# Kernel tuning notes

Measured on AMD Instinct MI355X. Metric: run time of the kernel, lower is better.

## Reference

```python
import jax, jax.numpy as jnp
import numpy as np

C = 256
GROUPS = 32
EPS = 1e-6


def setup_inputs() -> dict:
    key = jax.random.key(0)
    ks = jax.random.split(key, 11)
    b, c, h, w, d = 4, C, 16, 16, 16
    s = 0.02
    return {
        "x": jax.random.normal(ks[0], (b, c, h, w, d), jnp.float32),
        "gn_w": jnp.ones((c,), jnp.float32),
        "gn_b": jnp.zeros((c,), jnp.float32),
        "wq": jax.random.normal(ks[1], (c, c), jnp.float32) * s,
        "bq": jnp.zeros((c,), jnp.float32),
        "wk": jax.random.normal(ks[2], (c, c), jnp.float32) * s,
        "bk": jnp.zeros((c,), jnp.float32),
        "wv": jax.random.normal(ks[3], (c, c), jnp.float32) * s,
        "bv": jnp.zeros((c,), jnp.float32),
        "wo": jax.random.normal(ks[4], (c, c), jnp.float32) * s,
        "bo": jnp.zeros((c,), jnp.float32),
    }


def group_norm(x, w, b):
    bsz, c, h, wd, d = x.shape
    xg = x.reshape(bsz, GROUPS, c // GROUPS, h, wd, d)
    mean = xg.mean(axis=(2, 3, 4, 5), keepdims=True)
    var = xg.var(axis=(2, 3, 4, 5), keepdims=True)
    xg = (xg - mean) * jax.lax.rsqrt(var + EPS)
    x = xg.reshape(bsz, c, h, wd, d)
    return x * w[None, :, None, None, None] + b[None, :, None, None, None]


def conv1(x, w, b):
    # 1x1x1 conv == channel-mixing matmul; x: [b,c,h,w,d], w: [out,in]
    return jnp.einsum('oc,bchwd->bohwd', w, x) + b[None, :, None, None, None]


def reference(x, gn_w, gn_b, wq, bq, wk, bk, wv, bv, wo, bo):
    b, c, h, w, d = x.shape
    scale = c ** (-0.5)
    xn = group_norm(x, gn_w, gn_b)
    q = conv1(xn, wq, bq).reshape(b, c, h * w * d)
    k = conv1(xn, wk, bk).reshape(b, c, h * w * d)
    v = conv1(xn, wv, bv).reshape(b, c, h * w * d)
    attn = jnp.einsum('bci,bcj->bij', q, k) * scale  # [b, N, N]
    attn = jax.nn.softmax(attn, axis=2)
    out = jnp.einsum('bij,bcj->bci', attn, v).reshape(b, c, h, w, d)
    out = conv1(out, wo, bo)
    return x + out
```

## Files before the change

### kernel.cpp

```cpp
#include <hip/hip_runtime.h>
#include <hip/hip_bf16.h>

#define BB 4
#define CC 256
#define NN 4096
#define BBNN (BB * NN)
#define NGROUPS 32
#define CPG 8
#define EPSG 1e-6f
#define QKSCL 0.30028063f
#define KSPLIT 4
#define JITERS (NN / KSPLIT / 64)
#define KSTRIDE 272
#define DEFER_THR 8.0f

#define SIGMA(c) (((c) & 0xC0) | (((c) & 0x18) << 1) | (((c) & 0x20) >> 2) | ((c) & 7))

typedef __bf16 bf16x8 __attribute__((ext_vector_type(8)));
typedef float  f32x4  __attribute__((ext_vector_type(4)));

typedef __attribute__((address_space(1))) const void g_void;
typedef __attribute__((address_space(3))) void l_void;

__device__ __forceinline__ unsigned short f2bf(float f) {
  unsigned u = __builtin_bit_cast(unsigned, f);
  u += 0x7fffu + ((u >> 16) & 1u);
  return (unsigned short)(u >> 16);
}
__device__ __forceinline__ float bf2f(unsigned short s) {
  return __builtin_bit_cast(float, (unsigned)s << 16);
}

__device__ __forceinline__ f32x4 mfma16(bf16x8 a, bf16x8 b, f32x4 c) {
  return __builtin_amdgcn_mfma_f32_16x16x32_bf16(a, b, c, 0, 0, 0);
}
__device__ __forceinline__ f32x4 mfma8(long a, long b, f32x4 c) {
  return __builtin_amdgcn_mfma_f32_16x16x32_fp8_fp8(a, b, c, 0, 0, 0);
}

__device__ __forceinline__ bf16x8 ldfrag(const unsigned short* p) {
  return __builtin_bit_cast(bf16x8, *(const uint4*)p);
}

__global__ __launch_bounds__(256) void pre(const float* __restrict__ wq,
    const float* __restrict__ wk, const float* __restrict__ wv,
    const float* __restrict__ wo, const float* __restrict__ x,
    unsigned short* __restrict__ wbf, float* __restrict__ part) {
  if (blockIdx.x < 256) {
    int mat = blockIdx.x >> 6, blk = blockIdx.x & 63;
    const float* s = mat == 0 ? wq : mat == 1 ? wk : mat == 2 ? wv : wo;
    int i = (blk * 256 + threadIdx.x) * 4;
    float4 v = *(const float4*)&s[i];
    unsigned short* d = wbf + (size_t)mat * CC * CC + i;
    d[0] = f2bf(v.x); d[1] = f2bf(v.y); d[2] = f2bf(v.z); d[3] = f2bf(v.w);
    return;
  }
  int bx = blockIdx.x - 256;
  int pair = bx >> 1, h = bx & 1;
  const float* xp = x + (size_t)pair * (CPG * NN) + (size_t)h * (CPG * NN / 2);
  float s = 0.f, s2 = 0.f;
  for (int i = threadIdx.x; i < CPG * NN / 8; i += 256) {
    float4 v = ((const float4*)xp)[i];
    s += v.x + v.y + v.z + v.w;
    s2 += v.x * v.x + v.y * v.y + v.z * v.z + v.w * v.w;
  }
  for (int o = 32; o; o >>= 1) { s += __shfl_down(s, o); s2 += __shfl_down(s2, o); }
  __shared__ float rs[4], rs2[4];
  int wid = threadIdx.x >> 6, lane = threadIdx.x & 63;
  if (lane == 0) { rs[wid] = s; rs2[wid] = s2; }
  __syncthreads();
  if (threadIdx.x == 0) {
    part[bx * 2 + 0] = rs[0] + rs[1] + rs[2] + rs[3];
    part[bx * 2 + 1] = rs2[0] + rs2[1] + rs2[2] + rs2[3];
  }
}

__global__ __launch_bounds__(512) void gqkv(const float* __restrict__ x,
    const float* __restrict__ gw, const float* __restrict__ gb,
    const float* __restrict__ part, const unsigned short* __restrict__ wbf,
    const float* __restrict__ bq, const float* __restrict__ bk,
    const float* __restrict__ bv,
    unsigned char* __restrict__ q8, unsigned char* __restrict__ k8,
    unsigned char* __restrict__ v8) {
  const int low = blockIdx.x & 7;
  const int b = low & 3, shalf = low >> 2;
  const int u = blockIdx.x >> 3;
  const int sidx = (u >> 4) * 2 + shalf;
  const int nt = sidx * 16 + (u & 15);
  const int n0 = nt * 64;
  __shared__ unsigned short Xs[64][CC + 8];
  int tid = threadIdx.x;
  const float* xb = x + (size_t)b * CC * NN;
  {
    int item = tid;
    int g = item >> 4, nc = item & 15;
    int pair = b * NGROUPS + g;
    float s = part[pair * 4 + 0] + part[pair * 4 + 2];
    float s2 = part[pair * 4 + 1] + part[pair * 4 + 3];
    float mean = s / (CPG * NN);
    float inv = rsqrtf(s2 / (CPG * NN) - mean * mean + EPSG);
    unsigned short row[4][8];
#pragma unroll
    for (int cc = 0; cc < 8; ++cc) {
      int c = g * 8 + cc;
      float wv = gw[c];
      float scv = inv * wv;
      float biv = gb[c] - mean * scv;
      float4 v = *(const float4*)&xb[(size_t)c * NN + n0 + nc * 4];
      row[0][cc] = f2bf(v.x * scv + biv);
      row[1][cc] = f2bf(v.y * scv + biv);
      row[2][cc] = f2bf(v.z * scv + biv);
      row[3][cc] = f2bf(v.w * scv + biv);
    }
#pragma unroll
    for (int r = 0; r < 4; ++r)
      *(uint4*)&Xs[nc * 4 + r][g * 8] = *(const uint4*)&row[r][0];
  }
  __syncthreads();
  int w = tid >> 6, lane = tid & 63;
  int m = lane & 15, q4 = lane >> 4;
  int mode = w >> 2, wsub = w & 3;
  {
    bf16x8 xa[8];
#pragma unroll
    for (int k = 0; k < 8; ++k)
      xa[k] = ldfrag(&Xs[wsub * 16 + m][k * 32 + q4 * 8]);
    const unsigned short* W = wbf + (size_t)mode * CC * CC;
    const float* bias = mode ? bk : bq;
    unsigned char* dst = mode ? k8 : q8;
    for (int ot = 0; ot < 16; ++ot) {
      f32x4 acc = {0.f, 0.f, 0.f, 0.f};
#pragma unroll
      for (int k = 0; k < 8; ++k) {
        bf16x8 bf = ldfrag(&W[(size_t)(ot * 16 + m) * CC + k * 32 + q4 * 8]);
        acc = mfma16(xa[k], bf, acc);
      }
      int o = ot * 16 + m;
      int so = SIGMA(o);
      float bia = bias[o];
      unsigned pk01 = __builtin_amdgcn_cvt_pk_fp8_f32(
          (acc[0] + bia) * QKSCL, (acc[1] + bia) * QKSCL, 0u, false);
      unsigned pk23 = __builtin_amdgcn_cvt_pk_fp8_f32(
          (acc[2] + bia) * QKSCL, (acc[3] + bia) * QKSCL, 0u, false);
      size_t base = ((size_t)b * NN + n0 + wsub * 16 + q4 * 4) * CC + so;
      dst[base]          = (unsigned char)(pk01 & 0xff);
      dst[base + CC]     = (unsigned char)((pk01 >> 8) & 0xff);
      dst[base + 2 * CC] = (unsigned char)(pk23 & 0xff);
      dst[base + 3 * CC] = (unsigned char)((pk23 >> 8) & 0xff);
    }
  }
  {
    const unsigned short* Wv = wbf + 2 * CC * CC;
    int nthalf = w >> 2;
    for (int ot = 0; ot < 4; ++ot) {
      int o0 = (w & 3) * 64 + ot * 16;
      bf16x8 af[8];
#pragma unroll
      for (int k = 0; k < 8; ++k)
        af[k] = ldfrag(&Wv[(size_t)(o0 + m) * CC + k * 32 + q4 * 8]);
#pragma unroll
      for (int hh = 0; hh < 2; ++hh) {
        int nt4 = nthalf * 2 + hh;
        f32x4 acc = {0.f, 0.f, 0.f, 0.f};
#pragma unroll
        for (int k = 0; k < 8; ++k) {
          bf16x8 bfr = ldfrag(&Xs[nt4 * 16 + m][k * 32 + q4 * 8]);
          acc = mfma16(af[k], bfr, acc);
        }
        int j = nt4 * 16 + m;
        int jp = (j & 0x23) | ((j & 0x0C) << 1) | ((j & 0x10) >> 2);
        int n = n0 + jp;
        int o = o0 + q4 * 4;
        unsigned pk01 = __builtin_amdgcn_cvt_pk_fp8_f32(acc[0] + bv[o], acc[1] + bv[o + 1], 0u, false);
        unsigned pk23 = __builtin_amdgcn_cvt_pk_fp8_f32(acc[2] + bv[o + 2], acc[3] + bv[o + 3], 0u, false);
        size_t base = ((size_t)b * CC + o) * NN + n;
        v8[base]          = (unsigned char)(pk01 & 0xff);
        v8[base + NN]     = (unsigned char)((pk01 >> 8) & 0xff);
        v8[base + 2 * NN] = (unsigned char)(pk23 & 0xff);
        v8[base + 3 * NN] = (unsigned char)((pk23 >> 8) & 0xff);
      }
    }
  }
}

__device__ __forceinline__ void stageK8(const unsigned char* __restrict__ kp,
    int j0, unsigned char* Kb, int tid) {
#pragma unroll
  for (int t = 0; t < 4; ++t) {
    int item = t * 256 + tid;
    int row = item / 17, g = item % 17;
    int gs = (g == 16) ? 0 : g;
    const unsigned char* gp = kp + (size_t)(j0 + row) * CC + gs * 16;
    __builtin_amdgcn_global_load_lds((g_void*)gp, (l_void*)(Kb + item * 16), 16, 0, 0);
  }
  if (tid < 64) {
    int item = 1024 + tid;
    int row = item / 17, g = item % 17;
    int gs = (g == 16) ? 0 : g;
    const unsigned char* gp = kp + (size_t)(j0 + row) * CC + gs * 16;
    __builtin_amdgcn_global_load_lds((g_void*)gp, (l_void*)(Kb + item * 16), 16, 0, 0);
  }
}
__device__ __forceinline__ void stageV8(const unsigned char* __restrict__ vp,
    int j0, unsigned char* Vb, int tid) {
#pragma unroll
  for (int t = 0; t < 4; ++t) {
    int item = t * 256 + tid;
    int row = item >> 2, gl = item & 3;
    int gg = gl ^ (row & 3);
    const unsigned char* g = vp + (size_t)row * NN + j0 + gg * 16;
    __builtin_amdgcn_global_load_lds((g_void*)g, (l_void*)(Vb + item * 16), 16, 0, 0);
  }
}

__global__ __launch_bounds__(256, 2) void attn(const unsigned char* __restrict__ q8,
    const unsigned char* __restrict__ k8, const unsigned char* __restrict__ v8,
    unsigned short* __restrict__ accP, float* __restrict__ mlP) {
  const int grp = blockIdx.x & 15;
  const int s = grp >> 2, b = grp & 3;
  const int it = blockIdx.x >> 4;
  const int i0 = it * 128;
  __shared__ __align__(16) unsigned char pool[67584];
  unsigned char* Kd0 = pool;
  unsigned char* Kd1 = pool + 17408;
  unsigned char* Vd0 = pool + 34816;
  unsigned char* Vd1 = pool + 51200;
  int tid = threadIdx.x, w = tid >> 6, lane = tid & 63;
  int m = lane & 15, q4 = lane >> 4;
  int q4h = q4 >> 1, q4l = q4 & 1;
  const unsigned char* kp = k8 + (size_t)b * NN * CC;
  const unsigned char* vp = v8 + (size_t)b * CC * NN;
  const int iA0 = i0 + w * 32;
  long qaA[8], qaB[8];
#pragma unroll
  for (int t = 0; t < 4; ++t) {
    uint4 va = *(const uint4*)&q8[((size_t)b * NN + iA0 + m) * CC + t * 64 + q4 * 16];
    uint4 vb = *(const uint4*)&q8[((size_t)b * NN + iA0 + 16 + m) * CC + t * 64 + q4 * 16];
    uint2 alo = {va.x, va.y}, ahi = {va.z, va.w};
    uint2 blo = {vb.x, vb.y}, bhi = {vb.z, vb.w};
    qaA[2 * t]     = __builtin_bit_cast(long, alo);
    qaA[2 * t + 1] = __builtin_bit_cast(long, ahi);
    qaB[2 * t]     = __builtin_bit_cast(long, blo);
    qaB[2 * t + 1] = __builtin_bit_cast(long, bhi);
  }
  f32x4 accA[16], accB[16];
#pragma unroll
  for (int i = 0; i < 16; ++i) {
    accA[i] = (f32x4){0.f, 0.f, 0.f, 0.f};
    accB[i] = (f32x4){0.f, 0.f, 0.f, 0.f};
  }
  float mrowA = -1e30f, lrowA = 0.f, mrowB = -1e30f, lrowB = 0.f;
  const int jbase = s * (NN / KSPLIT);
  stageK8(kp, jbase, Kd0, tid);
  stageV8(vp, jbase, Vd0, tid);
  const unsigned char* Kbase0 = Kd0 + m * KSTRIDE + q4 * 16;
  const unsigned char* Kbase1 = Kd1 + m * KSTRIDE + q4 * 16;
  for (int jt = 0; jt < JITERS; ++jt) {
    __syncthreads();
    const unsigned char* Kbase = (jt & 1) ? Kbase1 : Kbase0;
    const unsigned char* Vs    = (jt & 1) ? Vd1 : Vd0;
    f32x4 svA[4], svB[4];
    __builtin_amdgcn_s_setprio(1);
#pragma unroll
    for (int jt4 = 0; jt4 < 4; ++jt4) {
      f32x4 aA = {0.f, 0.f, 0.f, 0.f};
      f32x4 aB = {0.f, 0.f, 0.f, 0.f};
#pragma unroll
      for (int c16 = 0; c16 < 4; ++c16) {
        uint4 kq = *(const uint4*)&Kbase[jt4 * 16 * KSTRIDE + c16 * 64];
        uint2 l2 = {kq.x, kq.y}, h2 = {kq.z, kq.w};
        long klo = __builtin_bit_cast(long, l2);
        long khi = __builtin_bit_cast(long, h2);
        aA = mfma8(klo, qaA[2 * c16], aA);
        aB = mfma8(klo, qaB[2 * c16], aB);
        aA = mfma8(khi, qaA[2 * c16 + 1], aA);
        aB = mfma8(khi, qaB[2 * c16 + 1], aB);
      }
      svA[jt4] = aA;
      svB[jt4] = aB;
    }
    __builtin_amdgcn_s_setprio(0);
    if (jt + 1 < JITERS) {
      stageK8(kp, jbase + (jt + 1) * 64, (jt & 1) ? Kd0 : Kd1, tid);
      stageV8(vp, jbase + (jt + 1) * 64, (jt & 1) ? Vd0 : Vd1, tid);
    }
    float mxA = -1e30f, mxB = -1e30f;
#pragma unroll
    for (int jt4 = 0; jt4 < 4; ++jt4) {
      mxA = fmaxf(mxA, fmaxf(fmaxf(svA[jt4][0], svA[jt4][1]), fmaxf(svA[jt4][2], svA[jt4][3])));
      mxB = fmaxf(mxB, fmaxf(fmaxf(svB[jt4][0], svB[jt4][1]), fmaxf(svB[jt4][2], svB[jt4][3])));
    }
    mxA = fmaxf(mxA, __shfl_xor(mxA, 16));
    mxA = fmaxf(mxA, __shfl_xor(mxA, 32));
    mxB = fmaxf(mxB, __shfl_xor(mxB, 16));
    mxB = fmaxf(mxB, __shfl_xor(mxB, 32));
    if (__any(mxA - mrowA > DEFER_THR)) {
      float mnewA = fmaxf(mrowA, mxA);
      float alphaA = exp2f(mrowA - mnewA);
      mrowA = mnewA;
      lrowA *= alphaA;
#pragma unroll
      for (int ct = 0; ct < 16; ++ct) accA[ct] *= alphaA;
    }
    if (__any(mxB - mrowB > DEFER_THR)) {
      float mnewB = fmaxf(mrowB, mxB);
      float alphaB = exp2f(mrowB - mnewB);
      mrowB = mnewB;
      lrowB *= alphaB;
#pragma unroll
      for (int ct = 0; ct < 16; ++ct) accB[ct] *= alphaB;
    }
    float rsumA = 0.f, rsumB = 0.f;
    unsigned pdA[4], pdB[4];
#pragma unroll
    for (int jt4 = 0; jt4 < 4; ++jt4) {
      float e0 = exp2f(svA[jt4][0] - mrowA);
      float e1 = exp2f(svA[jt4][1] - mrowA);
      float e2 = exp2f(svA[jt4][2] - mrowA);
      float e3 = exp2f(svA[jt4][3] - mrowA);
      rsumA += (e0 + e1) + (e2 + e3);
      unsigned d = __builtin_amdgcn_cvt_pk_fp8_f32(e0, e1, 0u, false);
      pdA[jt4] = __builtin_amdgcn_cvt_pk_fp8_f32(e2, e3, d, true);
      float f0 = exp2f(svB[jt4][0] - mrowB);
      float f1 = exp2f(svB[jt4][1] - mrowB);
      float f2 = exp2f(svB[jt4][2] - mrowB);
      float f3 = exp2f(svB[jt4][3] - mrowB);
      rsumB += (f0 + f1) + (f2 + f3);
      unsigned e = __builtin_amdgcn_cvt_pk_fp8_f32(f0, f1, 0u, false);
      pdB[jt4] = __builtin_amdgcn_cvt_pk_fp8_f32(f2, f3, e, true);
    }
    rsumA += __shfl_xor(rsumA, 16);
    rsumA += __shfl_xor(rsumA, 32);
    rsumB += __shfl_xor(rsumB, 16);
    rsumB += __shfl_xor(rsumB, 32);
    lrowA += rsumA;
    lrowB += rsumB;
    int voff = ((q4h) ^ (m & 3)) * 16 + q4l * 8;
    int voff1 = ((2 + q4h) ^ (m & 3)) * 16 + q4l * 8;
    __builtin_amdgcn_s_setprio(1);
#pragma unroll
    for (int p = 0; p < 2; ++p) {
      uint2 puA = {pdA[2 * p], pdA[2 * p + 1]};
      uint2 puB = {pdB[2 * p], pdB[2 * p + 1]};
      long pTA = __builtin_bit_cast(long, puA);
      long pTB = __builtin_bit_cast(long, puB);
      int vo = p ? voff1 : voff;
#pragma unroll
      for (int ct = 0; ct < 16; ++ct) {
        long vf = *(const long*)&Vs[(ct * 16 + m) * 64 + vo];
        accA[ct] = mfma8(vf, pTA, accA[ct]);
        accB[ct] = mfma8(vf, pTB, accB[ct]);
      }
    }
    __builtin_amdgcn_s_setprio(0);
  }
  size_t rqA = (size_t)(s * BB + b) * NN + iA0 + m;
  if (q4 == 0) {
    mlP[rqA * 2 + 0] = mrowA;
    mlP[rqA * 2 + 1] = lrowA;
    mlP[(rqA + 16) * 2 + 0] = mrowB;
    mlP[(rqA + 16) * 2 + 1] = lrowB;
  }
  __syncthreads();
  unsigned short* tp = (unsigned short*)pool;
#pragma unroll
  for (int half = 0; half < 2; ++half) {
    if ((w >> 1) == half) {
      int rbase = (w & 1) * 32;
#pragma unroll
      for (int ct = 0; ct < 16; ++ct) {
        unsigned loA = f2bf(accA[ct][0]) | ((unsigned)f2bf(accA[ct][1]) << 16);
        unsigned hiA = f2bf(accA[ct][2]) | ((unsigned)f2bf(accA[ct][3]) << 16);
        uint2 pkA = {loA, hiA};
        *(uint2*)&tp[(rbase + m) * 260 + ct * 16 + q4 * 4] = pkA;
        unsigned loB = f2bf(accB[ct][0]) | ((unsigned)f2bf(accB[ct][1]) << 16);
        unsigned hiB = f2bf(accB[ct][2]) | ((unsigned)f2bf(accB[ct][3]) << 16);
        uint2 pkB = {loB, hiB};
        *(uint2*)&tp[(rbase + 16 + m) * 260 + ct * 16 + q4 * 4] = pkB;
      }
    }
    __syncthreads();
#pragma unroll
    for (int u = 0; u < 8; ++u) {
      int id = u * 256 + tid;
      int row = id >> 5, ck = id & 31;
      uint4 v = *(const uint4*)&tp[row * 260 + ck * 8];
      *(uint4*)&accP[((size_t)(s * BB + b) * NN + i0 + half * 64 + row) * CC + ck * 8] = v;
    }
    __syncthreads();
  }
}

__global__ __launch_bounds__(256) void proj(const unsigned short* __restrict__ accP,
    const float* __restrict__ mlP, const unsigned short* __restrict__ Wo,
    const float* __restrict__ bo, const float* __restrict__ x,
    float* __restrict__ out) {
  const int b = blockIdx.x >> 7, nt = blockIdx.x & 127;
  const int n0 = nt * 32;
  __shared__ unsigned short As[32][CC + 8];
  __shared__ float wr[KSPLIT][36];
  int tid = threadIdx.x;
  if (tid < 32) {
    int n = n0 + tid;
    float mv[KSPLIT], lv[KSPLIT], M = -1e30f;
#pragma unroll
    for (int s = 0; s < KSPLIT; ++s) {
      size_t rq = (size_t)(s * BB + b) * NN + n;
      mv[s] = mlP[rq * 2];
      lv[s] = mlP[rq * 2 + 1];
      M = fmaxf(M, mv[s]);
    }
    float ws[KSPLIT], d = 0.f;
#pragma unroll
    for (int s = 0; s < KSPLIT; ++s) {
      ws[s] = exp2f(mv[s] - M);
      d += lv[s] * ws[s];
    }
    float inv = 1.f / d;
#pragma unroll
    for (int s = 0; s < KSPLIT; ++s) wr[s][tid] = ws[s] * inv;
  }
  __syncthreads();
#pragma unroll
  for (int i = 0; i < 4; ++i) {
    int id = tid + 256 * i;
    int r = id >> 5, ck = id & 31;
    int n = n0 + r;
    float f[8] = {0.f, 0.f, 0.f, 0.f, 0.f, 0.f, 0.f, 0.f};
#pragma unroll
    for (int s = 0; s < KSPLIT; ++s) {
      uint4 a = *(const uint4*)&accP[((size_t)(s * BB + b) * NN + n) * CC + ck * 8];
      const unsigned* p = (const unsigned*)&a;
      float wgt = wr[s][r];
#pragma unroll
      for (int k = 0; k < 4; ++k) {
        f[k * 2 + 0] += bf2f((unsigned short)(p[k] & 0xffff)) * wgt;
        f[k * 2 + 1] += bf2f((unsigned short)(p[k] >> 16)) * wgt;
      }
    }
    unsigned short ov[8];
#pragma unroll
    for (int k = 0; k < 8; ++k) ov[k] = f2bf(f[k]);
    *(uint4*)&As[r][ck * 8] = *(const uint4*)&ov[0];
  }
  __syncthreads();
  int w = tid >> 6, lane = tid & 63, m = lane & 15, q4 = lane >> 4;
  for (int ot = 0; ot < 4; ++ot) {
    int o0 = w * 64 + ot * 16;
    bf16x8 af[8];
#pragma unroll
    for (int k = 0; k < 8; ++k)
      af[k] = ldfrag(&Wo[(size_t)(o0 + m) * CC + k * 32 + q4 * 8]);
#pragma unroll
    for (int nt4 = 0; nt4 < 2; ++nt4) {
      f32x4 a = {0.f, 0.f, 0.f, 0.f};
#pragma unroll
      for (int k = 0; k < 8; ++k) {
        bf16x8 bf = ldfrag(&As[nt4 * 16 + m][k * 32 + q4 * 8]);
        a = mfma16(af[k], bf, a);
      }
      int n = n0 + nt4 * 16 + m;
#pragma unroll
      for (int r = 0; r < 4; ++r) {
        int o = o0 + q4 * 4 + r;
        size_t idx = ((size_t)b * CC + o) * NN + n;
        out[idx] = x[idx] + bo[o] + a[r];
      }
    }
  }
}

extern "C" void kernel_launch(void* const* d_in, const int* in_sizes, int n_in,
                              void* d_out, int out_size, void* d_ws, size_t ws_size,
                              hipStream_t stream) {
  const float* x  = (const float*)d_in[0];
  const float* gw = (const float*)d_in[1];
  const float* gb = (const float*)d_in[2];
  const float* wq = (const float*)d_in[3];
  const float* bq = (const float*)d_in[4];
  const float* wk = (const float*)d_in[5];
  const float* bk = (const float*)d_in[6];
  const float* wv = (const float*)d_in[7];
  const float* bv = (const float*)d_in[8];
  const float* wo = (const float*)d_in[9];
  const float* bo = (const float*)d_in[10];

  const size_t M4 = (size_t)BB * NN * CC;
  unsigned short* wbf = (unsigned short*)d_ws;
  unsigned short* accPb = wbf + 4 * CC * CC;
  float* mlP  = (float*)(accPb + (size_t)KSPLIT * M4);
  float* part = mlP + (size_t)KSPLIT * BBNN * 2;
  unsigned char* q8 = (unsigned char*)(part + 512);
  unsigned char* k8 = q8 + M4;
  unsigned char* v8 = k8 + M4;

  pre<<<512, 256, 0, stream>>>(wq, wk, wv, wo, x, wbf, part);
  gqkv<<<256, 512, 0, stream>>>(x, gw, gb, part, wbf, bq, bk, bv, q8, k8, v8);
  attn<<<KSPLIT * BB * 32, 256, 0, stream>>>(q8, k8, v8, accPb, mlP);
  proj<<<512, 256, 0, stream>>>(accPb, mlP, wbf + 3 * CC * CC, bo, x, (float*)d_out);
}
```

Baseline: 214.6 us.

## Software-pipeline PV matmul one tile behind QK with single K buffer

The attention loop now runs the P·V MFMAs for the previous key tile right after the QK^T MFMAs of the current tile, with a final PV step after the loop. The goal is to overlap the softmax exp and max work with matrix-core work instead of running them in series. K staging drops to one LDS buffer, which cuts shared memory from about 66 KB to about 49 KB and could allow more resident blocks. The cost is an extra __syncthreads per iteration and P fragments held live across iterations, which raises register pressure.

```diff
diff --git a/kernel.cpp b/kernel.cpp
--- a/kernel.cpp
+++ b/kernel.cpp
@@ -220,11 +220,10 @@
   const int s = grp >> 2, b = grp & 3;
   const int it = blockIdx.x >> 4;
   const int i0 = it * 128;
-  __shared__ __align__(16) unsigned char pool[67584];
-  unsigned char* Kd0 = pool;
-  unsigned char* Kd1 = pool + 17408;
-  unsigned char* Vd0 = pool + 34816;
-  unsigned char* Vd1 = pool + 51200;
+  __shared__ __align__(16) unsigned char pool[50176];
+  unsigned char* Kd  = pool;
+  unsigned char* Vd0 = pool + 17408;
+  unsigned char* Vd1 = pool + 33792;
   int tid = threadIdx.x, w = tid >> 6, lane = tid & 63;
   int m = lane & 15, q4 = lane >> 4;
   int q4h = q4 >> 1, q4l = q4 & 1;
@@ -251,14 +250,15 @@
   }
   float mrowA = -1e30f, lrowA = 0.f, mrowB = -1e30f, lrowB = 0.f;
   const int jbase = s * (NN / KSPLIT);
-  stageK8(kp, jbase, Kd0, tid);
+  stageK8(kp, jbase, Kd, tid);
   stageV8(vp, jbase, Vd0, tid);
-  const unsigned char* Kbase0 = Kd0 + m * KSTRIDE + q4 * 16;
-  const unsigned char* Kbase1 = Kd1 + m * KSTRIDE + q4 * 16;
+  const unsigned char* Kbase = Kd + m * KSTRIDE + q4 * 16;
+  const int voff  = ((q4h) ^ (m & 3)) * 16 + q4l * 8;
+  const int voff1 = ((2 + q4h) ^ (m & 3)) * 16 + q4l * 8;
+  unsigned pdA[4] = {0, 0, 0, 0}, pdB[4] = {0, 0, 0, 0};
   for (int jt = 0; jt < JITERS; ++jt) {
     __syncthreads();
-    const unsigned char* Kbase = (jt & 1) ? Kbase1 : Kbase0;
-    const unsigned char* Vs    = (jt & 1) ? Vd1 : Vd0;
+    const unsigned char* Vprev = (jt & 1) ? Vd0 : Vd1;
     f32x4 svA[4], svB[4];
     __builtin_amdgcn_s_setprio(1);
 #pragma unroll
@@ -279,10 +279,27 @@
       svA[jt4] = aA;
       svB[jt4] = aB;
     }
+    if (jt > 0) {
+#pragma unroll
+      for (int p = 0; p < 2; ++p) {
+        uint2 puA = {pdA[2 * p], pdA[2 * p + 1]};
+        uint2 puB = {pdB[2 * p], pdB[2 * p + 1]};
+        long pTA = __builtin_bit_cast(long, puA);
+        long pTB = __builtin_bit_cast(long, puB);
+        int vo = p ? voff1 : voff;
+#pragma unroll
+        for (int ct = 0; ct < 16; ++ct) {
+          long vf = *(const long*)&Vprev[(ct * 16 + m) * 64 + vo];
+          accA[ct] = mfma8(vf, pTA, accA[ct]);
+          accB[ct] = mfma8(vf, pTB, accB[ct]);
+        }
+      }
+    }
     __builtin_amdgcn_s_setprio(0);
+    __syncthreads();
     if (jt + 1 < JITERS) {
-      stageK8(kp, jbase + (jt + 1) * 64, (jt & 1) ? Kd0 : Kd1, tid);
-      stageV8(vp, jbase + (jt + 1) * 64, (jt & 1) ? Vd0 : Vd1, tid);
+      stageK8(kp, jbase + (jt + 1) * 64, Kd, tid);
+      stageV8(vp, jbase + (jt + 1) * 64, ((jt + 1) & 1) ? Vd1 : Vd0, tid);
     }
     float mxA = -1e30f, mxB = -1e30f;
 #pragma unroll
@@ -311,7 +328,6 @@
       for (int ct = 0; ct < 16; ++ct) accB[ct] *= alphaB;
     }
     float rsumA = 0.f, rsumB = 0.f;
-    unsigned pdA[4], pdB[4];
 #pragma unroll
     for (int jt4 = 0; jt4 < 4; ++jt4) {
       float e0 = exp2f(svA[jt4][0] - mrowA);
@@ -335,9 +351,9 @@
     rsumB += __shfl_xor(rsumB, 32);
     lrowA += rsumA;
     lrowB += rsumB;
-    int voff = ((q4h) ^ (m & 3)) * 16 + q4l * 8;
-    int voff1 = ((2 + q4h) ^ (m & 3)) * 16 + q4l * 8;
-    __builtin_amdgcn_s_setprio(1);
+  }
+  {
+    const unsigned char* Vlast = ((JITERS - 1) & 1) ? Vd1 : Vd0;
 #pragma unroll
     for (int p = 0; p < 2; ++p) {
       uint2 puA = {pdA[2 * p], pdA[2 * p + 1]};
@@ -347,12 +363,11 @@
       int vo = p ? voff1 : voff;
 #pragma unroll
       for (int ct = 0; ct < 16; ++ct) {
-        long vf = *(const long*)&Vs[(ct * 16 + m) * 64 + vo];
+        long vf = *(const long*)&Vlast[(ct * 16 + m) * 64 + vo];
         accA[ct] = mfma8(vf, pTA, accA[ct]);
         accB[ct] = mfma8(vf, pTB, accB[ct]);
       }
     }
-    __builtin_amdgcn_s_setprio(0);
   }
   size_t rqA = (size_t)(s * BB + b) * NN + iA0 + m;
   if (q4 == 0) {
```

Result: no change. 215.8 us (+0.6%).
